# Kernel tuning notes

Hardware: AMD Instinct MI355X
Metric: run time of the kernel (lower is better)

## Reference

```python
import jax, jax.numpy as jnp
import numpy as np
from math import sqrt

HEADS = 16
D_MODEL = 1024
HEAD_DIM = D_MODEL // HEADS  # 64
B, SEQ = 2, 2048


def setup_inputs() -> dict:
    key = jax.random.key(0)
    ks = jax.random.split(key, 8)
    k = jax.random.normal(ks[0], (B, SEQ, D_MODEL), dtype=jnp.float32)
    q = jax.random.normal(ks[1], (B, SEQ, D_MODEL), dtype=jnp.float32)
    v = jax.random.normal(ks[2], (B, SEQ, D_MODEL), dtype=jnp.float32)
    # causal mask, broadcast over batch and heads; masked_fill where mask == 0
    mask = jnp.tril(jnp.ones((SEQ, SEQ), dtype=jnp.int32))[None, None, :, :]
    s = 1.0 / sqrt(HEAD_DIM)
    Wq = jax.random.normal(ks[3], (HEAD_DIM, HEAD_DIM), dtype=jnp.float32) * s
    Wk = jax.random.normal(ks[4], (HEAD_DIM, HEAD_DIM), dtype=jnp.float32) * s
    Wv = jax.random.normal(ks[5], (HEAD_DIM, HEAD_DIM), dtype=jnp.float32) * s
    Wo = jax.random.normal(ks[6], (D_MODEL, D_MODEL), dtype=jnp.float32) * (1.0 / sqrt(D_MODEL))
    bo = jax.random.normal(ks[7], (D_MODEL,), dtype=jnp.float32) * 0.01
    return {"key": k, "query": q, "value": v, "mask": mask,
            "Wq": Wq, "Wk": Wk, "Wv": Wv, "Wo": Wo, "bo": bo}


def reference(key, query, value, mask, Wq, Wk, Wv, Wo, bo):
    b, q_len, d = query.shape
    k_len = key.shape[1]
    hd = d // HEADS
    # reshape to [b, len, heads, head_dim]
    k = key.reshape(b, k_len, HEADS, hd)
    q = query.reshape(b, q_len, HEADS, hd)
    v = value.reshape(b, k_len, HEADS, hd)
    # per-head-dim Linear (weights shared across heads); torch Linear: y = x @ W.T
    k = jnp.einsum('bkhd,ed->bkhe', k, Wk)
    q = jnp.einsum('bqhd,ed->bqhe', q, Wq)
    v = jnp.einsum('bvhd,ed->bvhe', v, Wv)
    # full attention matrix [b, h, q, k]
    product = jnp.einsum('bqhd,bkhd->bhqk', q, k)
    # NOTE: original masks BEFORE scaling by 1/sqrt(head_dim)
    product = jnp.where(mask == 0, jnp.float32(-1e20), product)
    product = product / jnp.float32(sqrt(hd))
    score = jax.nn.softmax(product, axis=-1)
    out = jnp.einsum('bhqv,bvhd->bqhd', score, v).reshape(b, q_len, d)
    out = out @ Wo.T + bo
    return out
```

## Files before the change

### kernel.cpp

```cpp
#include <hip/hip_runtime.h>

typedef __bf16 bf16x8 __attribute__((ext_vector_type(8)));
typedef float  f32x4  __attribute__((ext_vector_type(4)));
typedef float  f32x16 __attribute__((ext_vector_type(16)));
typedef unsigned int uint32x4 __attribute__((ext_vector_type(4)));

#define MFMA16(a, b, c) __builtin_amdgcn_mfma_f32_16x16x32_bf16((a), (b), (c), 0, 0, 0)
#define MFMA32(a, b, c) __builtin_amdgcn_mfma_f32_32x32x16_bf16((a), (b), (c), 0, 0, 0)

#define CVTPK(d, x, y) asm("v_cvt_pk_bf16_f32 %0, %1, %2" : "=v"(d) : "v"(x), "v"(y))
#define PLSWAP(a, b)   asm("v_permlane32_swap_b32 %0, %1" : "+v"(a), "+v"(b))

#define BAR_KEEP_VMEM() asm volatile("s_waitcnt lgkmcnt(0)\n\ts_barrier" ::: "memory")

__device__ inline float fast_exp2(float x) {
#if __has_builtin(__builtin_amdgcn_exp2f)
    return __builtin_amdgcn_exp2f(x);
#else
    return exp2f(x);
#endif
}

constexpr int SEQ = 2048;
constexpr int DM  = 1024;
constexpr int NH  = 16;
constexpr int HD  = 64;
constexpr int BATCH = 2;

__device__ inline bf16x8 ld8_f32(const float* p) {
    f32x4 a = *(const f32x4*)p;
    f32x4 b = *(const f32x4*)(p + 4);
    bf16x8 r;
    r[0] = (__bf16)a[0]; r[1] = (__bf16)a[1]; r[2] = (__bf16)a[2]; r[3] = (__bf16)a[3];
    r[4] = (__bf16)b[0]; r[5] = (__bf16)b[1]; r[6] = (__bf16)b[2]; r[7] = (__bf16)b[3];
    return r;
}

__global__ __launch_bounds__(256)
void proj_kernel(const float* __restrict__ Xq, const float* __restrict__ Xk,
                 const float* __restrict__ Xv,
                 const float* __restrict__ Wq, const float* __restrict__ Wk,
                 const float* __restrict__ Wv,
                 __bf16* __restrict__ Qp, __bf16* __restrict__ Kp,
                 __bf16* __restrict__ Vp)
{
    const int tid  = threadIdx.x;
    const int w    = tid >> 6;
    const int lane = tid & 63;
    const int quad = lane >> 4;
    const int l16  = lane & 15;
    const int sblk = blockIdx.x;
    const int bh   = blockIdx.y;
    const int tz   = blockIdx.z;

    const float* X = (tz == 0) ? Xq : (tz == 1) ? Xk : Xv;
    const float* W = (tz == 0) ? Wq : (tz == 1) ? Wk : Wv;
    __bf16*      O = (tz == 0) ? Qp : (tz == 1) ? Kp : Vp;
    const float scale = (tz == 0) ? (0.125f * 1.44269504088896f) : 1.0f;

    const int b = bh >> 4, h = bh & 15;
    const int mrow = sblk * 64 + w * 16 + l16;

    const size_t xoff = (size_t)(b * SEQ + mrow) * DM + h * HD + quad * 8;
    bf16x8 a0 = ld8_f32(X + xoff);
    bf16x8 a1 = ld8_f32(X + xoff + 32);

    f32x4 acc[4];
    #pragma unroll
    for (int nt = 0; nt < 4; ++nt) {
        const size_t woff = (size_t)(nt * 16 + l16) * HD + quad * 8;
        bf16x8 b0 = ld8_f32(W + woff);
        bf16x8 b1 = ld8_f32(W + woff + 32);
        f32x4 c = {0.f, 0.f, 0.f, 0.f};
        c = MFMA16(a0, b0, c);
        c = MFMA16(a1, b1, c);
        acc[nt] = c;
    }

    __bf16* obase = O + (size_t)bh * SEQ * HD;
    #pragma unroll
    for (int nt = 0; nt < 4; ++nt) {
        #pragma unroll
        for (int r = 0; r < 4; ++r) {
            const int srow = sblk * 64 + w * 16 + quad * 4 + r;
            obase[(size_t)srow * HD + nt * 16 + l16] = (__bf16)(acc[nt][r] * scale);
        }
    }
}

__global__ __launch_bounds__(256, 2)
void attn_kernel(const __bf16* __restrict__ Qp, const __bf16* __restrict__ Kp,
                 const __bf16* __restrict__ Vp, __bf16* __restrict__ AO)
{
    __shared__ __align__(16) unsigned int K_lds[2][64 * 36];
    __shared__ __align__(16) unsigned int VT2[2][64 * 36];

    const int tid  = threadIdx.x;
    const int w    = tid >> 6;
    const int lane = tid & 63;
    const int hi   = lane >> 5;
    const int l32  = lane & 31;
    const int qg   = w >> 1;
    const int kg   = w & 1;

    const int L   = blockIdx.x;
    const int pr  = (L >> 3) & 15;
    const int bh  = (L & 7) + 8 * (L >> 7);

    const __bf16* Qb = Qp + (size_t)bh * SEQ * HD;
    const __bf16* Kb = Kp + (size_t)bh * SEQ * HD;
    const __bf16* Vb = Vp + (size_t)bh * SEQ * HD;

    const int krow = tid >> 3, kcol = tid & 7;
    const int jp = tid & 31, d0 = (tid >> 5) * 8;

    #pragma unroll
    for (int phase = 0; phase < 2; ++phase) {
        const int tile = (phase == 0) ? (31 - pr) : pr;
        const int q0   = tile * 64;
        const int nkc  = tile + 1;

        __syncthreads();

        const __bf16* qp = Qb + (size_t)(q0 + 32 * qg + l32) * HD + hi * 8;
        const bf16x8 qb0 = *(const bf16x8*)(qp);
        const bf16x8 qb1 = *(const bf16x8*)(qp + 16);
        const bf16x8 qb2 = *(const bf16x8*)(qp + 32);
        const bf16x8 qb3 = *(const bf16x8*)(qp + 48);

        f32x16 accO[2];
        #pragma unroll
        for (int et = 0; et < 2; ++et) {
            #pragma unroll
            for (int r = 0; r < 16; ++r) accO[et][r] = 0.f;
        }
        float rs0 = 0.f, rs1 = 0.f;

        uint32x4 kA0, kA1, vAl, vAh, kB0, kB1, vBl, vBh;
        kA0 = *(const uint32x4*)(Kb + (size_t)krow * HD + kcol * 8);
        kA1 = *(const uint32x4*)(Kb + (size_t)(krow + 32) * HD + kcol * 8);
        vAl = *(const uint32x4*)(Vb + (size_t)(2 * jp) * HD + d0);
        vAh = *(const uint32x4*)(Vb + (size_t)(2 * jp + 1) * HD + d0);
        if (nkc > 1) {
            kB0 = *(const uint32x4*)(Kb + (size_t)(64 + krow) * HD + kcol * 8);
            kB1 = *(const uint32x4*)(Kb + (size_t)(64 + krow + 32) * HD + kcol * 8);
            vBl = *(const uint32x4*)(Vb + (size_t)(64 + 2 * jp) * HD + d0);
            vBh = *(const uint32x4*)(Vb + (size_t)(64 + 2 * jp + 1) * HD + d0);
        }

        auto STEP = [&](int kc, int buf, uint32x4& kp0, uint32x4& kp1,
                        uint32x4& vl, uint32x4& vh) {
            *(uint32x4*)&K_lds[buf][krow * 36 + kcol * 4]        = kp0;
            *(uint32x4*)&K_lds[buf][(krow + 32) * 36 + kcol * 4] = kp1;
            #pragma unroll
            for (int i2 = 0; i2 < 4; ++i2) {
                const unsigned int va = vl[i2], vb = vh[i2];
                VT2[buf][(d0 + 2 * i2    ) * 36 + jp] = (va & 0xffffu) | (vb << 16);
                VT2[buf][(d0 + 2 * i2 + 1) * 36 + jp] = (va >> 16) | (vb & 0xffff0000u);
            }

            if (kc + 2 < nkc) {
                const size_t o = (size_t)(kc + 2) * 64;
                kp0 = *(const uint32x4*)(Kb + (o + krow) * HD + kcol * 8);
                kp1 = *(const uint32x4*)(Kb + (o + krow + 32) * HD + kcol * 8);
                vl  = *(const uint32x4*)(Vb + (o + 2 * jp) * HD + d0);
                vh  = *(const uint32x4*)(Vb + (o + 2 * jp + 1) * HD + d0);
            }
            BAR_KEEP_VMEM();

            if (!(kc == tile && qg == 0 && kg == 1)) {
                const __bf16* kp = (const __bf16*)&K_lds[buf][(32 * kg + l32) * 36] + hi * 8;
                f32x16 s;
                #pragma unroll
                for (int r = 0; r < 16; ++r) s[r] = 0.f;
                s = MFMA32(*(const bf16x8*)(kp),      qb0, s);
                s = MFMA32(*(const bf16x8*)(kp + 16), qb1, s);
                s = MFMA32(*(const bf16x8*)(kp + 32), qb2, s);
                s = MFMA32(*(const bf16x8*)(kp + 48), qb3, s);

                if (kc == tile && qg == kg) {
                    #pragma unroll
                    for (int r = 0; r < 16; ++r) {
                        const int cr = (r & 3) + 8 * (r >> 2) + 4 * hi;
                        if (cr > l32) s[r] = -1e30f;
                    }
                }

                float p[16];
                #pragma unroll
                for (int r = 0; r < 16; ++r) p[r] = fast_exp2(s[r]);
                #pragma unroll
                for (int r = 0; r < 8; ++r) { rs0 += p[2 * r]; rs1 += p[2 * r + 1]; }

                unsigned int w0, w1, w2, w3, w4, w5, w6, w7;
                CVTPK(w0, p[0],  p[1]);  CVTPK(w1, p[2],  p[3]);
                CVTPK(w2, p[4],  p[5]);  CVTPK(w3, p[6],  p[7]);
                CVTPK(w4, p[8],  p[9]);  CVTPK(w5, p[10], p[11]);
                CVTPK(w6, p[12], p[13]); CVTPK(w7, p[14], p[15]);
                PLSWAP(w0, w2); PLSWAP(w1, w3); PLSWAP(w4, w6); PLSWAP(w5, w7);
                uint32x4 u0 = {w0, w1, w2, w3};
                uint32x4 u1 = {w4, w5, w6, w7};
                const bf16x8 pa0 = *(const bf16x8*)&u0;
                const bf16x8 pa1 = *(const bf16x8*)&u1;

                #pragma unroll
                for (int et = 0; et < 2; ++et) {
                    const __bf16* vp = (const __bf16*)&VT2[buf][(et * 32 + l32) * 36]
                                       + 32 * kg + hi * 8;
                    accO[et] = MFMA32(pa0, *(const bf16x8*)(vp),      accO[et]);
                    accO[et] = MFMA32(pa1, *(const bf16x8*)(vp + 16), accO[et]);
                }
            }
        };

        for (int kc = 0; kc < nkc; kc += 2) {
            STEP(kc, 0, kA0, kA1, vAl, vAh);
            if (kc + 1 < nkc) STEP(kc + 1, 1, kB0, kB1, vBl, vBh);
        }

        __syncthreads();
        float* red = (float*)K_lds;
        float rsum = rs0 + rs1;
        if (kg == 1) {
            float* dst = red + (size_t)(qg * 64 + lane) * 33;
            #pragma unroll
            for (int r = 0; r < 16; ++r) { dst[r] = accO[0][r]; dst[16 + r] = accO[1][r]; }
            dst[32] = rsum;
        }
        __syncthreads();
        if (kg == 0) {
            const float* src = red + (size_t)(qg * 64 + lane) * 33;
            #pragma unroll
            for (int r = 0; r < 16; ++r) { accO[0][r] += src[r]; accO[1][r] += src[16 + r]; }
            rsum += src[32];
            const float rt  = rsum + __shfl_xor(rsum, 32, 64);
            const float ivq = 1.0f / rt;
            const int b = bh >> 4, h = bh & 15;
            #pragma unroll
            for (int r = 0; r < 16; ++r) {
                const int cr = (r & 3) + 8 * (r >> 2) + 4 * hi;
                const float iv = __shfl(ivq, cr, 64);
                __bf16* ao = AO + (size_t)(b * SEQ + q0 + 32 * qg + cr) * DM + h * HD;
                ao[l32]      = (__bf16)(accO[0][r] * iv);
                ao[32 + l32] = (__bf16)(accO[1][r] * iv);
            }
        }
    }
}

__global__ __launch_bounds__(256)
void wconv_kernel(const float* __restrict__ Wo, __bf16* __restrict__ Wb)
{
    const size_t i = ((size_t)blockIdx.x * 256 + threadIdx.x) * 8;
    *(bf16x8*)(Wb + i) = ld8_f32(Wo + i);
}

__global__ __launch_bounds__(256)
void ogemm_kernel(const __bf16* __restrict__ AO, const __bf16* __restrict__ Wb,
                  const float* __restrict__ bo, float* __restrict__ out)
{
    __shared__ __align__(16) unsigned int A_lds[2][64 * 36];
    __shared__ __align__(16) unsigned int B_lds[2][128 * 36];

    const int tid  = threadIdx.x;
    const int w    = tid >> 6;
    const int lane = tid & 63;
    const int quad = lane >> 4;
    const int l16  = lane & 15;
    const int m0   = blockIdx.x * 64;
    const int n0   = blockIdx.y * 128;

    const int row = tid >> 3, c = tid & 7;

    f32x4 acc[8];
    #pragma unroll
    for (int nt = 0; nt < 8; ++nt) { f32x4 z = {0.f,0.f,0.f,0.f}; acc[nt] = z; }

    uint32x4 aA[2], bA[4], aB[2], bB[4];
    #pragma unroll
    for (int i = 0; i < 2; ++i) {
        aA[i] = *(const uint32x4*)(AO + (size_t)(m0 + row + i * 32) * DM + c * 8);
        aB[i] = *(const uint32x4*)(AO + (size_t)(m0 + row + i * 32) * DM + 64 + c * 8);
    }
    #pragma unroll
    for (int i = 0; i < 4; ++i) {
        bA[i] = *(const uint32x4*)(Wb + (size_t)(n0 + row + i * 32) * DM + c * 8);
        bB[i] = *(const uint32x4*)(Wb + (size_t)(n0 + row + i * 32) * DM + 64 + c * 8);
    }

    auto GSTEP = [&](int kc, int buf, uint32x4 (&ap)[2], uint32x4 (&bp)[4]) {
        #pragma unroll
        for (int i = 0; i < 2; ++i)
            *(uint32x4*)&A_lds[buf][(row + i * 32) * 36 + c * 4] = ap[i];
        #pragma unroll
        for (int i = 0; i < 4; ++i)
            *(uint32x4*)&B_lds[buf][(row + i * 32) * 36 + c * 4] = bp[i];

        if (kc + 2 < DM / 64) {
            const size_t o = (size_t)(kc + 2) * 64;
            #pragma unroll
            for (int i = 0; i < 2; ++i)
                ap[i] = *(const uint32x4*)(AO + (size_t)(m0 + row + i * 32) * DM + o + c * 8);
            #pragma unroll
            for (int i = 0; i < 4; ++i)
                bp[i] = *(const uint32x4*)(Wb + (size_t)(n0 + row + i * 32) * DM + o + c * 8);
        }
        BAR_KEEP_VMEM();

        #pragma unroll
        for (int ks = 0; ks < 2; ++ks) {
            bf16x8 a = *(const bf16x8*)&A_lds[buf][(w * 16 + l16) * 36 + ks * 16 + quad * 4];
            #pragma unroll
            for (int nt = 0; nt < 8; ++nt) {
                bf16x8 bb = *(const bf16x8*)&B_lds[buf][(nt * 16 + l16) * 36 + ks * 16 + quad * 4];
                acc[nt] = MFMA16(a, bb, acc[nt]);
            }
        }
    };

    for (int kc = 0; kc < DM / 64; kc += 2) {
        GSTEP(kc,     0, aA, bA);
        GSTEP(kc + 1, 1, aB, bB);
    }

    #pragma unroll
    for (int nt = 0; nt < 8; ++nt) {
        const int n = n0 + nt * 16 + l16;
        const float bof = bo[n];
        #pragma unroll
        for (int r = 0; r < 4; ++r) {
            const int m = m0 + w * 16 + quad * 4 + r;
            out[(size_t)m * DM + n] = acc[nt][r] + bof;
        }
    }
}

extern "C" void kernel_launch(void* const* d_in, const int* in_sizes, int n_in,
                              void* d_out, int out_size, void* d_ws, size_t ws_size,
                              hipStream_t stream)
{
    const float* key   = (const float*)d_in[0];
    const float* query = (const float*)d_in[1];
    const float* value = (const float*)d_in[2];
    const float* Wq = (const float*)d_in[4];
    const float* Wk = (const float*)d_in[5];
    const float* Wv = (const float*)d_in[6];
    const float* Wo = (const float*)d_in[7];
    const float* bo = (const float*)d_in[8];

    const size_t per = (size_t)BATCH * NH * SEQ * HD;
    __bf16* Qp = (__bf16*)d_ws;
    __bf16* Kp = Qp + per;
    __bf16* Vp = Kp + per;
    __bf16* AO = Vp + per;
    __bf16* Wb = Kp;

    proj_kernel<<<dim3(SEQ / 64, BATCH * NH, 3), 256, 0, stream>>>(
        query, key, value, Wq, Wk, Wv, Qp, Kp, Vp);
    attn_kernel<<<dim3(16 * BATCH * NH), 256, 0, stream>>>(Qp, Kp, Vp, AO);
    wconv_kernel<<<dim3(DM * DM / (256 * 8)), 256, 0, stream>>>(Wo, Wb);
    ogemm_kernel<<<dim3(BATCH * SEQ / 64, DM / 128), 256, 0, stream>>>(
        AO, Wb, bo, (float*)d_out);
}
```

Before: 186.1 us.

## Process two key chunks per barrier with 128-row double-buffered LDS tiles

The attention loop now stages 128 keys (two 64-key chunks) of K and transposed V into LDS per iteration, with double buffering, and runs two compute sub-steps per barrier. This halves the number of block-wide barriers and issues larger batches of global loads per iteration. In exchange LDS use doubles (about 72KB per block), which may limit occupancy to fewer than the two blocks per CU set in the launch bounds. Prefetch registers also double and the prefetch distance shrinks from two chunks to one large tile.

```diff
diff --git a/kernel.cpp b/kernel.cpp
--- a/kernel.cpp
+++ b/kernel.cpp
@@ -92,8 +92,8 @@
 void attn_kernel(const __bf16* __restrict__ Qp, const __bf16* __restrict__ Kp,
                  const __bf16* __restrict__ Vp, __bf16* __restrict__ AO)
 {
-    __shared__ __align__(16) unsigned int K_lds[2][64 * 36];
-    __shared__ __align__(16) unsigned int VT2[2][64 * 36];
+    __shared__ __align__(16) unsigned int K_lds[2][128 * 36];
+    __shared__ __align__(16) unsigned int VT2[2][128 * 36];
 
     const int tid  = threadIdx.x;
     const int w    = tid >> 6;
@@ -119,6 +119,7 @@
         const int tile = (phase == 0) ? (31 - pr) : pr;
         const int q0   = tile * 64;
         const int nkc  = tile + 1;
+        const int nbig = (nkc + 1) >> 1;
 
         __syncthreads();
 
@@ -136,86 +137,87 @@
         }
         float rs0 = 0.f, rs1 = 0.f;
 
-        uint32x4 kA0, kA1, vAl, vAh, kB0, kB1, vBl, vBh;
-        kA0 = *(const uint32x4*)(Kb + (size_t)krow * HD + kcol * 8);
-        kA1 = *(const uint32x4*)(Kb + (size_t)(krow + 32) * HD + kcol * 8);
-        vAl = *(const uint32x4*)(Vb + (size_t)(2 * jp) * HD + d0);
-        vAh = *(const uint32x4*)(Vb + (size_t)(2 * jp + 1) * HD + d0);
-        if (nkc > 1) {
-            kB0 = *(const uint32x4*)(Kb + (size_t)(64 + krow) * HD + kcol * 8);
-            kB1 = *(const uint32x4*)(Kb + (size_t)(64 + krow + 32) * HD + kcol * 8);
-            vBl = *(const uint32x4*)(Vb + (size_t)(64 + 2 * jp) * HD + d0);
-            vBh = *(const uint32x4*)(Vb + (size_t)(64 + 2 * jp + 1) * HD + d0);
-        }
-
-        auto STEP = [&](int kc, int buf, uint32x4& kp0, uint32x4& kp1,
-                        uint32x4& vl, uint32x4& vh) {
-            *(uint32x4*)&K_lds[buf][krow * 36 + kcol * 4]        = kp0;
-            *(uint32x4*)&K_lds[buf][(krow + 32) * 36 + kcol * 4] = kp1;
-            #pragma unroll
-            for (int i2 = 0; i2 < 4; ++i2) {
-                const unsigned int va = vl[i2], vb = vh[i2];
-                VT2[buf][(d0 + 2 * i2    ) * 36 + jp] = (va & 0xffffu) | (vb << 16);
-                VT2[buf][(d0 + 2 * i2 + 1) * 36 + jp] = (va >> 16) | (vb & 0xffff0000u);
-            }
-
-            if (kc + 2 < nkc) {
-                const size_t o = (size_t)(kc + 2) * 64;
-                kp0 = *(const uint32x4*)(Kb + (o + krow) * HD + kcol * 8);
-                kp1 = *(const uint32x4*)(Kb + (o + krow + 32) * HD + kcol * 8);
-                vl  = *(const uint32x4*)(Vb + (o + 2 * jp) * HD + d0);
-                vh  = *(const uint32x4*)(Vb + (o + 2 * jp + 1) * HD + d0);
+        uint32x4 kpre[4], vpre[4];
+        #pragma unroll
+        for (int s2 = 0; s2 < 2; ++s2) {
+            kpre[2*s2]   = *(const uint32x4*)(Kb + (size_t)(s2*64 + krow) * HD + kcol * 8);
+            kpre[2*s2+1] = *(const uint32x4*)(Kb + (size_t)(s2*64 + krow + 32) * HD + kcol * 8);
+            vpre[2*s2]   = *(const uint32x4*)(Vb + (size_t)(s2*64 + 2*jp) * HD + d0);
+            vpre[2*s2+1] = *(const uint32x4*)(Vb + (size_t)(s2*64 + 2*jp + 1) * HD + d0);
+        }
+
+        auto COMPUTE = [&](int kc, int buf, int sub) {
+            if (kc == tile && qg == 0 && kg == 1) return;
+            const __bf16* kp = (const __bf16*)&K_lds[buf][(sub*64 + 32*kg + l32) * 36] + hi * 8;
+            f32x16 s;
+            #pragma unroll
+            for (int r = 0; r < 16; ++r) s[r] = 0.f;
+            s = MFMA32(*(const bf16x8*)(kp),      qb0, s);
+            s = MFMA32(*(const bf16x8*)(kp + 16), qb1, s);
+            s = MFMA32(*(const bf16x8*)(kp + 32), qb2, s);
+            s = MFMA32(*(const bf16x8*)(kp + 48), qb3, s);
+
+            if (kc == tile && qg == kg) {
+                #pragma unroll
+                for (int r = 0; r < 16; ++r) {
+                    const int cr = (r & 3) + 8 * (r >> 2) + 4 * hi;
+                    if (cr > l32) s[r] = -1e30f;
+                }
+            }
+
+            float p[16];
+            #pragma unroll
+            for (int r = 0; r < 16; ++r) p[r] = fast_exp2(s[r]);
+            #pragma unroll
+            for (int r = 0; r < 8; ++r) { rs0 += p[2 * r]; rs1 += p[2 * r + 1]; }
+
+            unsigned int w0, w1, w2, w3, w4, w5, w6, w7;
+            CVTPK(w0, p[0],  p[1]);  CVTPK(w1, p[2],  p[3]);
+            CVTPK(w2, p[4],  p[5]);  CVTPK(w3, p[6],  p[7]);
+            CVTPK(w4, p[8],  p[9]);  CVTPK(w5, p[10], p[11]);
+            CVTPK(w6, p[12], p[13]); CVTPK(w7, p[14], p[15]);
+            PLSWAP(w0, w2); PLSWAP(w1, w3); PLSWAP(w4, w6); PLSWAP(w5, w7);
+            uint32x4 u0 = {w0, w1, w2, w3};
+            uint32x4 u1 = {w4, w5, w6, w7};
+            const bf16x8 pa0 = *(const bf16x8*)&u0;
+            const bf16x8 pa1 = *(const bf16x8*)&u1;
+
+            #pragma unroll
+            for (int et = 0; et < 2; ++et) {
+                const __bf16* vp = (const __bf16*)&VT2[buf][(sub*64 + et*32 + l32) * 36]
+                                   + 32 * kg + hi * 8;
+                accO[et] = MFMA32(pa0, *(const bf16x8*)(vp),      accO[et]);
+                accO[et] = MFMA32(pa1, *(const bf16x8*)(vp + 16), accO[et]);
+            }
+        };
+
+        for (int t = 0; t < nbig; ++t) {
+            const int buf = t & 1;
+            #pragma unroll
+            for (int s2 = 0; s2 < 2; ++s2) {
+                *(uint32x4*)&K_lds[buf][(s2*64 + krow) * 36 + kcol * 4]      = kpre[2*s2];
+                *(uint32x4*)&K_lds[buf][(s2*64 + krow + 32) * 36 + kcol * 4] = kpre[2*s2+1];
+                #pragma unroll
+                for (int i2 = 0; i2 < 4; ++i2) {
+                    const unsigned int va = vpre[2*s2][i2], vb = vpre[2*s2+1][i2];
+                    VT2[buf][(s2*64 + d0 + 2*i2    ) * 36 + jp] = (va & 0xffffu) | (vb << 16);
+                    VT2[buf][(s2*64 + d0 + 2*i2 + 1) * 36 + jp] = (va >> 16) | (vb & 0xffff0000u);
+                }
+            }
+            if (t + 1 < nbig) {
+                const size_t o = (size_t)(t + 1) * 128;
+                #pragma unroll
+                for (int s2 = 0; s2 < 2; ++s2) {
+                    kpre[2*s2]   = *(const uint32x4*)(Kb + (o + s2*64 + krow) * HD + kcol * 8);
+                    kpre[2*s2+1] = *(const uint32x4*)(Kb + (o + s2*64 + krow + 32) * HD + kcol * 8);
+                    vpre[2*s2]   = *(const uint32x4*)(Vb + (o + s2*64 + 2*jp) * HD + d0);
+                    vpre[2*s2+1] = *(const uint32x4*)(Vb + (o + s2*64 + 2*jp + 1) * HD + d0);
+                }
             }
             BAR_KEEP_VMEM();
 
-            if (!(kc == tile && qg == 0 && kg == 1)) {
-                const __bf16* kp = (const __bf16*)&K_lds[buf][(32 * kg + l32) * 36] + hi * 8;
-                f32x16 s;
-                #pragma unroll
-                for (int r = 0; r < 16; ++r) s[r] = 0.f;
-                s = MFMA32(*(const bf16x8*)(kp),      qb0, s);
-                s = MFMA32(*(const bf16x8*)(kp + 16), qb1, s);
-                s = MFMA32(*(const bf16x8*)(kp + 32), qb2, s);
-                s = MFMA32(*(const bf16x8*)(kp + 48), qb3, s);
-
-                if (kc == tile && qg == kg) {
-                    #pragma unroll
-                    for (int r = 0; r < 16; ++r) {
-                        const int cr = (r & 3) + 8 * (r >> 2) + 4 * hi;
-                        if (cr > l32) s[r] = -1e30f;
-                    }
-                }
-
-                float p[16];
-                #pragma unroll
-                for (int r = 0; r < 16; ++r) p[r] = fast_exp2(s[r]);
-                #pragma unroll
-                for (int r = 0; r < 8; ++r) { rs0 += p[2 * r]; rs1 += p[2 * r + 1]; }
-
-                unsigned int w0, w1, w2, w3, w4, w5, w6, w7;
-                CVTPK(w0, p[0],  p[1]);  CVTPK(w1, p[2],  p[3]);
-                CVTPK(w2, p[4],  p[5]);  CVTPK(w3, p[6],  p[7]);
-                CVTPK(w4, p[8],  p[9]);  CVTPK(w5, p[10], p[11]);
-                CVTPK(w6, p[12], p[13]); CVTPK(w7, p[14], p[15]);
-                PLSWAP(w0, w2); PLSWAP(w1, w3); PLSWAP(w4, w6); PLSWAP(w5, w7);
-                uint32x4 u0 = {w0, w1, w2, w3};
-                uint32x4 u1 = {w4, w5, w6, w7};
-                const bf16x8 pa0 = *(const bf16x8*)&u0;
-                const bf16x8 pa1 = *(const bf16x8*)&u1;
-
-                #pragma unroll
-                for (int et = 0; et < 2; ++et) {
-                    const __bf16* vp = (const __bf16*)&VT2[buf][(et * 32 + l32) * 36]
-                                       + 32 * kg + hi * 8;
-                    accO[et] = MFMA32(pa0, *(const bf16x8*)(vp),      accO[et]);
-                    accO[et] = MFMA32(pa1, *(const bf16x8*)(vp + 16), accO[et]);
-                }
-            }
-        };
-
-        for (int kc = 0; kc < nkc; kc += 2) {
-            STEP(kc, 0, kA0, kA1, vAl, vAh);
-            if (kc + 1 < nkc) STEP(kc + 1, 1, kB0, kB1, vBl, vBh);
+            COMPUTE(2*t, buf, 0);
+            if (2*t + 1 < nkc) COMPUTE(2*t + 1, buf, 1);
         }
 
         __syncthreads();
```

After: 186.1 us. Within noise of the previous version (+0.0%).
